# Kernel tuning notes

Measured on AMD Instinct MI355X. Metric: run time of the kernel, lower is better.

The kernel has to match this reference:

```python
import jax, jax.numpy as jnp
import numpy as np

N_NODES = 50000
N_EDGES = 800000
NUM_FEATURES = 128
HIDDEN = 128
NUM_CLASSES = 10
NUM_GRAPHS = 512
PROCESSING_STEPS = 4


def setup_inputs() -> dict:
    key = jax.random.key(0)
    ks = jax.random.split(key, 20)
    s = 0.05
    inp = {
        'x': jax.random.normal(ks[0], (N_NODES, NUM_FEATURES), jnp.float32),
        'edge_index': jax.random.randint(ks[1], (2, N_EDGES), 0, N_NODES),
        'batch': jnp.sort(jax.random.randint(ks[2], (N_NODES,), 0, NUM_GRAPHS)),
        # GCN layers (weights stored [in, out])
        'W1': jax.random.normal(ks[3], (NUM_FEATURES, HIDDEN), jnp.float32) * s,
        'b1': jnp.zeros((HIDDEN,), jnp.float32),
        'W2': jax.random.normal(ks[4], (HIDDEN, HIDDEN), jnp.float32) * s,
        'b2': jnp.zeros((HIDDEN,), jnp.float32),
        'W3': jax.random.normal(ks[5], (HIDDEN, HIDDEN), jnp.float32) * s,
        'b3': jnp.zeros((HIDDEN,), jnp.float32),
        # Set2Set LSTM cell: input 2*HIDDEN -> hidden HIDDEN, torch gate order i,f,g,o
        'Wih': jax.random.normal(ks[6], (4 * HIDDEN, 2 * HIDDEN), jnp.float32) * s,
        'Whh': jax.random.normal(ks[7], (4 * HIDDEN, HIDDEN), jnp.float32) * s,
        'bih': jnp.zeros((4 * HIDDEN,), jnp.float32),
        'bhh': jnp.zeros((4 * HIDDEN,), jnp.float32),
        # MLP head
        'L1w': jax.random.normal(ks[8], (2 * HIDDEN, HIDDEN), jnp.float32) * s,
        'L1b': jnp.zeros((HIDDEN,), jnp.float32),
        'L2w': jax.random.normal(ks[9], (HIDDEN, HIDDEN // 2), jnp.float32) * s,
        'L2b': jnp.zeros((HIDDEN // 2,), jnp.float32),
        'L3w': jax.random.normal(ks[10], (HIDDEN // 2, NUM_CLASSES), jnp.float32) * s,
        'L3b': jnp.zeros((NUM_CLASSES,), jnp.float32),
    }
    return inp


def _gcn_conv(x, row, col, W, b, n):
    # PyG GCNConv: x @ W, symmetric normalization with self-loops, scatter-add to targets.
    xw = x @ W  # [N, out]
    deg = jax.ops.segment_sum(jnp.ones_like(col, dtype=xw.dtype), col, num_segments=n)
    dis = jnp.where(deg > 0, jax.lax.rsqrt(jnp.maximum(deg, 1.0)), 0.0)
    norm = dis[row] * dis[col]  # [E+N]
    out = jax.ops.segment_sum(norm[:, None] * xw[row], col, num_segments=n)
    return out + b


def _segment_softmax(e, batch, n_seg):
    emax = jax.lax.stop_gradient(jax.ops.segment_max(e, batch, num_segments=n_seg))
    emax = jnp.where(jnp.isfinite(emax), emax, 0.0)
    a = jnp.exp(e - emax[batch])
    asum = jax.ops.segment_sum(a, batch, num_segments=n_seg)
    return a / jnp.where(asum > 0, asum, 1.0)[batch]


def reference(x, edge_index, batch, W1, b1, W2, b2, W3, b3,
              Wih, Whh, bih, bhh, L1w, L1b, L2w, L2b, L3w, L3b):
    n = x.shape[0]
    # add self loops once
    loops = jnp.arange(n, dtype=edge_index.dtype)
    row = jnp.concatenate([edge_index[0], loops])  # sources
    col = jnp.concatenate([edge_index[1], loops])  # targets

    h = jax.nn.relu(_gcn_conv(x, row, col, W1, b1, n))
    h = jax.nn.relu(_gcn_conv(h, row, col, W2, b2, n))
    h = jax.nn.relu(_gcn_conv(h, row, col, W3, b3, n))

    # Set2Set readout (processing_steps=4)
    d = h.shape[1]
    hs = jnp.zeros((NUM_GRAPHS, d), h.dtype)
    cs = jnp.zeros((NUM_GRAPHS, d), h.dtype)
    q_star = jnp.zeros((NUM_GRAPHS, 2 * d), h.dtype)
    for _ in range(PROCESSING_STEPS):
        gates = q_star @ Wih.T + hs @ Whh.T + bih + bhh  # [B, 4d]
        ig, fg, gg, og = jnp.split(gates, 4, axis=-1)
        cs = jax.nn.sigmoid(fg) * cs + jax.nn.sigmoid(ig) * jnp.tanh(gg)
        q = jax.nn.sigmoid(og) * jnp.tanh(cs)
        hs = q
        e = jnp.sum(h * q[batch], axis=-1)  # [N]
        a = _segment_softmax(e, batch, NUM_GRAPHS)
        r = jax.ops.segment_sum(a[:, None] * h, batch, num_segments=NUM_GRAPHS)
        q_star = jnp.concatenate([q, r], axis=-1)

    # MLP head (dropout inactive in eval)
    y = jax.nn.relu(q_star @ L1w + L1b)
    y = jax.nn.relu(y @ L2w + L2b)
    y = y @ L3w + L3b
    return jax.nn.log_softmax(y, axis=-1)
```

## Files before the change

kernel.cpp:

```cpp
#include <hip/hip_runtime.h>

constexpr int NN  = 50000;
constexpr int NE  = 800000;
constexpr int FD  = 128;
constexpr int NG  = 512;
constexpr int NB  = 4;
constexpr int BCAP = 24;
constexpr int CAP = NB * BCAP;
constexpr int SLICE = 12500;
constexpr int NBKT   = 196;
constexpr int BNODES = 256;
constexpr int CAPB   = 6144;

typedef __attribute__((ext_vector_type(8))) short bf16x8;
typedef __attribute__((ext_vector_type(4))) float f32x4;

__device__ __forceinline__ float bf2f(unsigned short u) {
    unsigned int v = ((unsigned int)u) << 16;
    float f; __builtin_memcpy(&f, &v, 4); return f;
}
__device__ __forceinline__ unsigned short f2bf(float f) {
    unsigned int u; __builtin_memcpy(&u, &f, 4);
    u += 0x7FFFu + ((u >> 16) & 1u);
    return (unsigned short)(u >> 16);
}
__device__ __forceinline__ float2 bfp(unsigned int u) {
    unsigned int lo = u << 16, hi = u & 0xFFFF0000u;
    float2 r; __builtin_memcpy(&r.x, &lo, 4); __builtin_memcpy(&r.y, &hi, 4);
    return r;
}
__device__ __forceinline__ unsigned int packbf(float a, float b) {
    return (unsigned int)f2bf(a) | ((unsigned int)f2bf(b) << 16);
}
__device__ __forceinline__ float sigmoidf(float x) { return 1.0f / (1.0f + __expf(-x)); }
__device__ __forceinline__ float ldw(const void* p, int idx, int flag) {
    return flag ? ((const float*)p)[idx] : bf2f(((const unsigned short*)p)[idx]);
}

__global__ void k_detect(const unsigned int* __restrict__ xw, int* __restrict__ flag,
                         int* __restrict__ gcnt) {
    if (threadIdx.x < NBKT) gcnt[threadIdx.x] = 0;
    __shared__ int cnt;
    if (threadIdx.x == 0) cnt = 0;
    __syncthreads();
    int local = 0;
    for (int i = threadIdx.x; i < 2048; i += 256) {
        unsigned int w = xw[i];
        unsigned int h0 = w & 0xFFFFu, h1 = w >> 16;
        if (((h0 >> 7) & 0xFF) >= 0x90) local++;
        if (((h1 >> 7) & 0xFF) >= 0x90) local++;
    }
    atomicAdd(&cnt, local);
    __syncthreads();
    if (threadIdx.x == 0) *flag = (cnt > 256) ? 1 : 0;
}

__global__ void k_cvt_x(const void* __restrict__ src, unsigned short* __restrict__ dst,
                        const int* __restrict__ batch, int* __restrict__ goff,
                        const int* __restrict__ flagp) {
    int i = blockIdx.x * 256 + threadIdx.x;
    if (i < NN * FD / 8) {
        if (*flagp) {
            const float4* s = (const float4*)src;
            float4 a = s[2 * i], b = s[2 * i + 1];
            uint4 o;
            o.x = packbf(a.x, a.y); o.y = packbf(a.z, a.w);
            o.z = packbf(b.x, b.y); o.w = packbf(b.z, b.w);
            ((uint4*)dst)[i] = o;
        } else {
            ((uint4*)dst)[i] = ((const uint4*)src)[i];
        }
    }
    if (i < NN) {
        int b = batch[i];
        if (b < 0) b = 0;
        if (b >= NG) b = NG - 1;
        int prev;
        if (i == 0) prev = -1;
        else {
            prev = batch[i - 1];
            if (prev < 0) prev = 0;
            if (prev >= NG) prev = NG - 1;
        }
        for (int g = prev + 1; g <= b; g++) goff[g] = i;
        if (i == NN - 1)
            for (int g = b + 1; g <= NG; g++) goff[g] = NN;
    }
}

struct WDesc {
    const void* src[12];
    void* dst[12];
    int kind[12];
    int off[13];
};
__global__ void k_cvt_w(WDesc d, const int* __restrict__ flagp) {
    int gid = blockIdx.x * 256 + threadIdx.x;
    if (gid >= d.off[12]) return;
    int flag = *flagp;
    int t = 0;
    while (gid >= d.off[t + 1]) t++;
    int i = gid - d.off[t];
    if (d.kind[t] == 0) {
        if (flag) ((unsigned short*)d.dst[t])[i] = f2bf(((const float*)d.src[t])[i]);
        else      ((unsigned short*)d.dst[t])[i] = ((const unsigned short*)d.src[t])[i];
    } else {
        int n = i >> 6, k2 = i & 63;
        ((unsigned int*)d.dst[t])[i] = packbf(ldw(d.src[t], (2 * k2) * 128 + n, flag),
                                              ldw(d.src[t], (2 * k2 + 1) * 128 + n, flag));
    }
}

__global__ void k_wt(const void* __restrict__ Wih, const void* __restrict__ Whh,
                     const void* __restrict__ bih, const void* __restrict__ bhh,
                     unsigned int* __restrict__ WcombT,
                     unsigned int* __restrict__ WrT,
                     float* __restrict__ bsum, const int* __restrict__ flagp) {
    int gid = blockIdx.x * 256 + threadIdx.x;
    int flag = *flagp;
    if (gid < 64 * 512) {
        int k2 = gid >> 9, row = gid & 511;
        float a0 = ldw(Wih, row * 256 + 2 * k2, flag)     + ldw(Whh, row * 128 + 2 * k2, flag);
        float a1 = ldw(Wih, row * 256 + 2 * k2 + 1, flag) + ldw(Whh, row * 128 + 2 * k2 + 1, flag);
        WcombT[(k2 >> 1) * 1024 + 2 * row + (k2 & 1)] = packbf(a0, a1);
    } else if (gid < 2 * 64 * 512) {
        int g2 = gid - 64 * 512;
        int k2 = g2 >> 9, row = g2 & 511;
        WrT[(k2 >> 1) * 1024 + 2 * row + (k2 & 1)] =
            packbf(ldw(Wih, row * 256 + 128 + 2 * k2, flag),
                   ldw(Wih, row * 256 + 128 + 2 * k2 + 1, flag));
    } else if (gid < 2 * 64 * 512 + 512) {
        int row = gid - 2 * 64 * 512;
        bsum[row] = ldw(bih, row, flag) + ldw(bhh, row, flag);
    }
}

__global__ __launch_bounds__(256) void k_fill1(const int* __restrict__ ei,
                                               int* __restrict__ gcnt,
                                               unsigned int* __restrict__ bktbuf) {
    __shared__ int hist[NBKT];
    __shared__ int wbase[NBKT];
    int t = threadIdx.x;
    for (int i = t; i < NBKT; i += 256) hist[i] = 0;
    __syncthreads();
    int base_e = blockIdx.x * 2048;
    int bb[8], rk[8];
    unsigned int pk[8];
#pragma unroll
    for (int k = 0; k < 8; k++) {
        int e = base_e + k * 256 + t;
        if (e < NE) {
            int r = ei[e], c = ei[NE + e];
            if ((unsigned)r >= (unsigned)NN) r = 0;
            if ((unsigned)c >= (unsigned)NN) c = 0;
            bb[k] = c >> 8;
            rk[k] = atomicAdd(&hist[bb[k]], 1);
            pk[k] = ((unsigned)c << 16) | (unsigned)r;
        } else bb[k] = -1;
    }
    __syncthreads();
    for (int i = t; i < NBKT; i += 256)
        wbase[i] = hist[i] ? atomicAdd(&gcnt[i], hist[i]) : 0;
    __syncthreads();
#pragma unroll
    for (int k = 0; k < 8; k++) {
        if (bb[k] >= 0) {
            int pos = wbase[bb[k]] + rk[k];
            if (pos < CAPB) bktbuf[bb[k] * CAPB + pos] = pk[k];
        }
    }
}

__global__ __launch_bounds__(512) void k_fill2(const unsigned int* __restrict__ bktbuf,
                                               const int* __restrict__ gcnt,
                                               int* __restrict__ bcnt,
                                               unsigned short* __restrict__ csr_row) {
    int b = blockIdx.x, t = threadIdx.x;
    __shared__ int lcnt[BNODES * NB];
    for (int i = t; i < BNODES * NB; i += 512) lcnt[i] = 0;
    uint4* creg = (uint4*)(csr_row + (size_t)b * BNODES * CAP);
    for (int i = t; i < BNODES * CAP / 8; i += 512)
        creg[i] = (uint4){0, 0, 0, 0};
    __syncthreads();
    int n = gcnt[b]; if (n > CAPB) n = CAPB;
    const unsigned int* bp = bktbuf + (size_t)b * CAPB;
    for (int i = t; i < n; i += 512) {
        unsigned int v = bp[i];
        int r = v & 0xFFFFu;
        int c = v >> 16;
        int cl = c & (BNODES - 1);
        int nb = r / SLICE;
        int pos = atomicAdd(&lcnt[cl * NB + nb], 1);
        if (pos < BCAP)
            csr_row[(size_t)c * CAP + nb * BCAP + pos] = (unsigned short)r;
    }
    __syncthreads();
    for (int i = t; i < BNODES * NB; i += 512) {
        int node = b * BNODES + (i >> 2);
        if (node < NN) bcnt[(size_t)node * NB + (i & 3)] = lcnt[i];
    }
}

__global__ __launch_bounds__(256) void k_gemm(const unsigned short* __restrict__ H,
                                              const unsigned int* __restrict__ WT,
                                              const int4* __restrict__ bcnt4,
                                              unsigned short* __restrict__ XW, int M) {
    __shared__ alignas(16) unsigned short WB[128 * 136];
    int t = threadIdx.x;
    unsigned int* WBu = (unsigned int*)WB;
    for (int c = t; c < 2048; c += 256) {
        uint4 v = ((const uint4*)WT)[c];
        int n = c >> 4, k2q = c & 15;
        *(uint4*)(WBu + n * 68 + k2q * 4) = v;
    }
    __syncthreads();
    int wave = t >> 6, lane = t & 63;
    int lm = lane & 15;
    int lq = lane >> 4;
    int row = blockIdx.x * 64 + wave * 16 + lm;
    int rowc = (row < M) ? row : (M - 1);
    const unsigned short* Arow = H + (size_t)rowc * 128;
    f32x4 acc[8];
#pragma unroll
    for (int n = 0; n < 8; n++) acc[n] = (f32x4){0.f, 0.f, 0.f, 0.f};
#pragma unroll
    for (int kk = 0; kk < 4; kk++) {
        bf16x8 afrag = *(const bf16x8*)(Arow + kk * 32 + lq * 8);
        const unsigned short* wbase = WB + kk * 32 + lq * 8;
#pragma unroll
        for (int n = 0; n < 8; n++) {
            bf16x8 bfrag = *(const bf16x8*)(wbase + (n * 16 + lm) * 136);
            acc[n] = __builtin_amdgcn_mfma_f32_16x16x32_bf16(afrag, bfrag, acc[n], 0, 0, 0);
        }
    }
    __syncthreads();
#pragma unroll
    for (int r = 0; r < 4; r++) {
        int row_local = wave * 16 + lq * 4 + r;
        int orow = blockIdx.x * 64 + row_local;
        int oc = (orow < M) ? orow : (M - 1);
        int4 bc = bcnt4[oc];
        float dn = rsqrtf((float)(bc.x + bc.y + bc.z + bc.w + 1));
#pragma unroll
        for (int n = 0; n < 8; n++)
            WB[row_local * 136 + n * 16 + lm] = f2bf(acc[n][r] * dn);
    }
#pragma unroll
    for (int it = 0; it < 4; it++) {
        int row_local = wave * 16 + it * 4 + (lane >> 4);
        int row_global = blockIdx.x * 64 + row_local;
        uint4 v = *(const uint4*)(WB + row_local * 136 + (lane & 15) * 8);
        if (row_global < M)
            *((uint4*)(XW + (size_t)row_global * 128) + (lane & 15)) = v;
    }
}

__global__ __launch_bounds__(256) void k_aggr(const unsigned short* __restrict__ XW,
                                              const int4* __restrict__ bcnt4,
                                              const unsigned short* __restrict__ csr_row,
                                              const unsigned short* __restrict__ bias,
                                              unsigned short* __restrict__ Hout) {
    int wave = threadIdx.x >> 6;
    int lane = threadIdx.x & 63;
    int nsel = lane >> 4;
    int sub  = lane & 15;
    int node = blockIdx.x * 16 + wave * 4 + nsel;
    if (node >= NN) return;
    const uint4* XW4 = (const uint4*)XW;
    int4 bc = bcnt4[node];
    int deg = bc.x + bc.y + bc.z + bc.w;
    float dn = rsqrtf((float)(deg + 1));
    uint4 sv = XW4[(size_t)node * 16 + sub];
    float2 s0 = bfp(sv.x), s1 = bfp(sv.y), s2 = bfp(sv.z), s3 = bfp(sv.w);
    float a0 = s0.x, a1 = s0.y, a2 = s1.x, a3 = s1.y;
    float a4 = s2.x, a5 = s2.y, a6 = s3.x, a7 = s3.y;
    int cnts[NB] = {bc.x, bc.y, bc.z, bc.w};
    const unsigned short* lst = csr_row + (size_t)node * CAP;
#pragma unroll
    for (int b = 0; b < NB; b++) {
        int n = cnts[b]; if (n > BCAP) n = BCAP;
        const unsigned short* lb = lst + b * BCAP;
        int j = 0;
        for (; j + 4 <= n; j += 4) {
            int r0 = lb[j], r1 = lb[j + 1], r2 = lb[j + 2], r3 = lb[j + 3];
            uint4 v0 = XW4[(size_t)r0 * 16 + sub];
            uint4 v1 = XW4[(size_t)r1 * 16 + sub];
            uint4 v2 = XW4[(size_t)r2 * 16 + sub];
            uint4 v3 = XW4[(size_t)r3 * 16 + sub];
            float2 f;
            f = bfp(v0.x); a0 += f.x; a1 += f.y;
            f = bfp(v0.y); a2 += f.x; a3 += f.y;
            f = bfp(v0.z); a4 += f.x; a5 += f.y;
            f = bfp(v0.w); a6 += f.x; a7 += f.y;
            f = bfp(v1.x); a0 += f.x; a1 += f.y;
            f = bfp(v1.y); a2 += f.x; a3 += f.y;
            f = bfp(v1.z); a4 += f.x; a5 += f.y;
            f = bfp(v1.w); a6 += f.x; a7 += f.y;
            f = bfp(v2.x); a0 += f.x; a1 += f.y;
            f = bfp(v2.y); a2 += f.x; a3 += f.y;
            f = bfp(v2.z); a4 += f.x; a5 += f.y;
            f = bfp(v2.w); a6 += f.x; a7 += f.y;
            f = bfp(v3.x); a0 += f.x; a1 += f.y;
            f = bfp(v3.y); a2 += f.x; a3 += f.y;
            f = bfp(v3.z); a4 += f.x; a5 += f.y;
            f = bfp(v3.w); a6 += f.x; a7 += f.y;
        }
        for (; j < n; j++) {
            int r = lb[j];
            uint4 v = XW4[(size_t)r * 16 + sub];
            float2 f;
            f = bfp(v.x); a0 += f.x; a1 += f.y;
            f = bfp(v.y); a2 += f.x; a3 += f.y;
            f = bfp(v.z); a4 += f.x; a5 += f.y;
            f = bfp(v.w); a6 += f.x; a7 += f.y;
        }
    }
    uint4 bv = ((const uint4*)bias)[sub];
    float2 b0 = bfp(bv.x), b1 = bfp(bv.y), b2 = bfp(bv.z), b3 = bfp(bv.w);
    uint4 o;
    o.x = packbf(fmaxf(dn * a0 + b0.x, 0.0f), fmaxf(dn * a1 + b0.y, 0.0f));
    o.y = packbf(fmaxf(dn * a2 + b1.x, 0.0f), fmaxf(dn * a3 + b1.y, 0.0f));
    o.z = packbf(fmaxf(dn * a4 + b2.x, 0.0f), fmaxf(dn * a5 + b2.y, 0.0f));
    o.w = packbf(fmaxf(dn * a6 + b3.x, 0.0f), fmaxf(dn * a7 + b3.y, 0.0f));
    ((uint4*)Hout)[(size_t)node * 16 + sub] = o;
}

__global__ __launch_bounds__(512) void k_s2s(const unsigned short* __restrict__ H,
                                             const int* __restrict__ goff,
                                             const unsigned int* __restrict__ WcombT,
                                             const unsigned int* __restrict__ WrT,
                                             const float* __restrict__ bsum,
                                             const unsigned short* __restrict__ L1w,
                                             const unsigned short* __restrict__ L1b,
                                             const unsigned short* __restrict__ L2w,
                                             const unsigned short* __restrict__ L2b,
                                             const unsigned short* __restrict__ L3w,
                                             const unsigned short* __restrict__ L3b,
                                             void* __restrict__ out,
                                             const int* __restrict__ flagp) {
    int g = blockIdx.x, t = threadIdx.x;
    __shared__ float qsr[256];
    __shared__ float hsv[128], csv[128];
    __shared__ float gates[512];
    __shared__ float wred[8];
    __shared__ float wrr[8][128];
    __shared__ float ps[128];
    __shared__ float qrep[4 * 132];
    __shared__ float y1[128], y2[64], y3[10], lseS[1];

    if (t < 256) qsr[t] = 0.0f;
    if (t < 128) { hsv[t] = 0.0f; csv[t] = 0.0f; }
    __syncthreads();

    int s = goff[g], e = goff[g + 1];
    if (s < 0) s = 0;
    if (e > NN) e = NN;
    if (e < s) e = s;
    int w = t >> 6, lane = t & 63;
    const unsigned int* Hu = (const unsigned int*)H;

    int nq = t >> 2;
    int fq = (t & 3) * 16;
    const float* qc = qrep + (t & 3) * 132 + 2 * fq;
    const uint2* WC2 = (const uint2*)WcombT;
    const uint2* WR2 = (const uint2*)WrT;

    for (int step = 0; step < 4; step++) {
        {
            float accA = bsum[t], accB = 0.0f, accC = 0.0f, accD = 0.0f;
#pragma unroll 8
            for (int p = 0; p < 32; p++) {
                uint2 u = WC2[p * 512 + t];
                float2 w0 = bfp(u.x), w1 = bfp(u.y);
                accA += w0.x * hsv[4 * p];     accB += w0.y * hsv[4 * p + 1];
                accC += w1.x * hsv[4 * p + 2]; accD += w1.y * hsv[4 * p + 3];
            }
#pragma unroll 8
            for (int p = 0; p < 32; p++) {
                uint2 u = WR2[p * 512 + t];
                float2 w0 = bfp(u.x), w1 = bfp(u.y);
                accA += w0.x * qsr[128 + 4 * p];     accB += w0.y * qsr[128 + 4 * p + 1];
                accC += w1.x * qsr[128 + 4 * p + 2]; accD += w1.y * qsr[128 + 4 * p + 3];
            }
            gates[t] = (accA + accB) + (accC + accD);
        }
        __syncthreads();
        if (t < 128) {
            float ig = sigmoidf(gates[t]),       fg = sigmoidf(gates[128 + t]);
            float gg = tanhf(gates[256 + t]),    og = sigmoidf(gates[384 + t]);
            float c = fg * csv[t] + ig * gg;
            float q = og * tanhf(c);
            csv[t] = c;
            hsv[t] = q;
            qsr[t] = q;
            qrep[t] = q; qrep[132 + t] = q; qrep[264 + t] = q; qrep[396 + t] = q;
        }
        __syncthreads();

        float m = -1e30f, l = 0.0f, r0 = 0.0f, r1 = 0.0f;
        for (int cs = s; cs < e; cs += 128) {
            int ce = cs + 128; if (ce > e) ce = e;
            int nid = cs + nq;
            float eacc = 0.0f;
            if (nid < ce) {
                const unsigned int* hrow = Hu + (size_t)nid * 64 + fq;
#pragma unroll
                for (int u = 0; u < 16; u += 4) {
                    uint4 hv = *(const uint4*)(hrow + u);
                    float2 f0 = bfp(hv.x), f1 = bfp(hv.y);
                    float2 f2 = bfp(hv.z), f3 = bfp(hv.w);
                    const float* qp = qc + 2 * u;
                    eacc += f0.x * qp[0] + f0.y * qp[1] + f1.x * qp[2] + f1.y * qp[3]
                          + f2.x * qp[4] + f2.y * qp[5] + f3.x * qp[6] + f3.y * qp[7];
                }
            }
            eacc += __shfl_xor(eacc, 1);
            eacc += __shfl_xor(eacc, 2);
            float esc = (nid < ce) ? eacc : -1e30f;
            float vmax = esc;
            for (int d = 4; d < 64; d <<= 1) vmax = fmaxf(vmax, __shfl_xor(vmax, d));
            if (lane == 0) wred[w] = vmax;
            __syncthreads();
            float M = m;
#pragma unroll
            for (int k = 0; k < 8; k++) M = fmaxf(M, wred[k]);
            float p = __expf(esc - M);
            bool lead = ((t & 3) == 0) && (nid < ce);
            if (lead) ps[nq] = p;
            float psum = lead ? p : 0.0f;
            for (int d = 1; d < 64; d <<= 1) psum += __shfl_xor(psum, d);
            __syncthreads();
            if (lane == 0) wred[w] = psum;
            __syncthreads();
            float Lc = 0.0f;
#pragma unroll
            for (int k = 0; k < 8; k++) Lc += wred[k];
            float scale = __expf(m - M);
            l = l * scale + Lc;
            r0 *= scale; r1 *= scale;
            m = M;
            int i = cs + w;
            for (; i + 24 < ce; i += 32) {
                float p0 = ps[i - cs],      p1 = ps[i + 8 - cs];
                float p2 = ps[i + 16 - cs], p3 = ps[i + 24 - cs];
                unsigned int v0 = Hu[(size_t)i * 64 + lane];
                unsigned int v1 = Hu[(size_t)(i + 8) * 64 + lane];
                unsigned int v2 = Hu[(size_t)(i + 16) * 64 + lane];
                unsigned int v3 = Hu[(size_t)(i + 24) * 64 + lane];
                float2 f0 = bfp(v0), f1 = bfp(v1), f2 = bfp(v2), f3 = bfp(v3);
                r0 += p0 * f0.x + p1 * f1.x + p2 * f2.x + p3 * f3.x;
                r1 += p0 * f0.y + p1 * f1.y + p2 * f2.y + p3 * f3.y;
            }
            for (; i < ce; i += 8) {
                float p0 = ps[i - cs];
                float2 f = bfp(Hu[(size_t)i * 64 + lane]);
                r0 += p0 * f.x; r1 += p0 * f.y;
            }
            __syncthreads();
        }
        wrr[w][2 * lane]     = r0;
        wrr[w][2 * lane + 1] = r1;
        __syncthreads();
        if (t < 128) {
            float R = 0.0f;
#pragma unroll
            for (int k = 0; k < 8; k++) R += wrr[k][t];
            float L = l;
            if (!(L > 0.0f)) L = 1.0f;
            qsr[128 + t] = R / L;
        }
        __syncthreads();
    }

    if (t < 128) {
        float acc = bf2f(L1b[t]);
        for (int i = 0; i < 256; i++) acc += bf2f(L1w[i * 128 + t]) * qsr[i];
        y1[t] = fmaxf(acc, 0.0f);
    }
    __syncthreads();
    if (t < 64) {
        float a2 = bf2f(L2b[t]);
        for (int i = 0; i < 128; i++) a2 += bf2f(L2w[i * 64 + t]) * y1[i];
        y2[t] = fmaxf(a2, 0.0f);
    }
    __syncthreads();
    if (t < 10) {
        float a3 = bf2f(L3b[t]);
        for (int i = 0; i < 64; i++) a3 += bf2f(L3w[i * 10 + t]) * y2[i];
        y3[t] = a3;
    }
    __syncthreads();
    if (t == 0) {
        float m = y3[0];
        for (int i = 1; i < 10; i++) m = fmaxf(m, y3[i]);
        float s2 = 0.0f;
        for (int i = 0; i < 10; i++) s2 += __expf(y3[i] - m);
        lseS[0] = m + __logf(s2);
    }
    __syncthreads();
    if (t < 10) {
        float v = y3[t] - lseS[0];
        if (!(v == v)) v = -9.0f;
        if (*flagp) ((float*)out)[g * 10 + t] = v;
        else        ((unsigned short*)out)[g * 10 + t] = f2bf(v);
    }
}

extern "C" void kernel_launch(void* const* d_in, const int* in_sizes, int n_in,
                              void* d_out, int out_size, void* d_ws, size_t ws_size,
                              hipStream_t stream) {
    const int* ei  = (const int*)d_in[1];
    const int* bat = (const int*)d_in[2];

    char* base = (char*)d_ws;
    size_t woff = 0;
    auto alloc = [&](size_t bytes) -> void* {
        void* r = base + woff;
        woff = (woff + bytes + 255) & ~(size_t)255;
        return r;
    };
    unsigned short* A = (unsigned short*)alloc((size_t)NN * FD * 2);
    unsigned short* B = (unsigned short*)alloc((size_t)NN * FD * 2);
    unsigned short* csr_row = (unsigned short*)alloc((size_t)NBKT * BNODES * CAP * 2);
    int*   bcnt     = (int*)alloc((size_t)NN * NB * 4);
    int*   goff     = (int*)alloc((NG + 1) * 4);
    int*   flag     = (int*)alloc(256);
    int*   gcnt     = (int*)alloc(NBKT * 4);
    unsigned int* WcombT = (unsigned int*)alloc(64 * 512 * 4);
    unsigned int* WrT    = (unsigned int*)alloc(64 * 512 * 4);
    float* bsum          = (float*)alloc(512 * 4);
    unsigned int* cWT1 = (unsigned int*)alloc(8192 * 4);
    unsigned int* cWT2 = (unsigned int*)alloc(8192 * 4);
    unsigned int* cWT3 = (unsigned int*)alloc(8192 * 4);
    auto walloc = [&](int n) { return (unsigned short*)alloc((size_t)n * 2); };
    unsigned short* cb1  = walloc(128);
    unsigned short* cb2  = walloc(128);
    unsigned short* cb3  = walloc(128);
    unsigned short* cL1w = walloc(256 * 128);
    unsigned short* cL1b = walloc(128);
    unsigned short* cL2w = walloc(128 * 64);
    unsigned short* cL2b = walloc(64);
    unsigned short* cL3w = walloc(64 * 10);
    unsigned short* cL3b = walloc(10);
    unsigned int* bktbuf = (unsigned int*)A;
    (void)ws_size; (void)in_sizes; (void)n_in; (void)out_size;

    k_detect<<<1, 256, 0, stream>>>((const unsigned int*)d_in[0], flag, gcnt);
    k_cvt_x<<<(NN * FD / 8 + 255) / 256, 256, 0, stream>>>(d_in[0], B, bat, goff, flag);
    {
        WDesc d;
        const int idxs[12]  = {3,    4,  5,    6,  7,    8,  13, 14, 15, 16, 17, 18};
        void* dsts[12]      = {cWT1, cb1, cWT2, cb2, cWT3, cb3,
                               cL1w, cL1b, cL2w, cL2b, cL3w, cL3b};
        const int kinds[12] = {1, 0, 1, 0, 1, 0, 0, 0, 0, 0, 0, 0};
        const int ns[12]    = {8192, 128, 8192, 128, 8192, 128,
                               256 * 128, 128, 128 * 64, 64, 64 * 10, 10};
        int acc = 0;
        for (int i = 0; i < 12; i++) {
            d.src[i] = d_in[idxs[i]];
            d.dst[i] = dsts[i];
            d.kind[i] = kinds[i];
            d.off[i] = acc;
            acc += ns[i];
        }
        d.off[12] = acc;
        k_cvt_w<<<(acc + 255) / 256, 256, 0, stream>>>(d, flag);
    }
    k_wt<<<(2 * 64 * 512 + 512 + 255) / 256, 256, 0, stream>>>(
        d_in[9], d_in[10], d_in[11], d_in[12], WcombT, WrT, bsum, flag);

    k_fill1<<<(NE + 2047) / 2048, 256, 0, stream>>>(ei, gcnt, bktbuf);
    k_fill2<<<NBKT, 512, 0, stream>>>(bktbuf, gcnt, bcnt, csr_row);

    const int gemmBlk = (NN + 63) / 64;
    const int aggrBlk = (NN + 15) / 16;

    k_gemm<<<gemmBlk, 256, 0, stream>>>(B, cWT1, (const int4*)bcnt, A, NN);
    k_aggr<<<aggrBlk, 256, 0, stream>>>(A, (const int4*)bcnt, csr_row, cb1, B);
    k_gemm<<<gemmBlk, 256, 0, stream>>>(B, cWT2, (const int4*)bcnt, A, NN);
    k_aggr<<<aggrBlk, 256, 0, stream>>>(A, (const int4*)bcnt, csr_row, cb2, B);
    k_gemm<<<gemmBlk, 256, 0, stream>>>(B, cWT3, (const int4*)bcnt, A, NN);
    k_aggr<<<aggrBlk, 256, 0, stream>>>(A, (const int4*)bcnt, csr_row, cb3, B);

    k_s2s<<<NG, 512, 0, stream>>>(B, goff, WcombT, WrT, bsum,
                                  cL1w, cL1b, cL2w, cL2b, cL3w, cL3b,
                                  d_out, flag);
}
```

Baseline: 319.9 us.

## Merge weight-conversion kernels, cache LSTM weights in registers, trim s2s barriers

Folds the k_cvt_w weight conversion into k_wt so one launch does both, saving a kernel launch. In the Set2Set kernel, 24 of the 32 combined-gate weight vectors are held in registers across the four processing steps instead of being reloaded from global memory each step. The softmax max and sum reductions now use separate shared slots, which removes one barrier, and the trailing barrier in the chunk loop runs only when another chunk follows. The register caching raises register pressure at 512 threads per block, which may cost occupancy.

Result: slower. 336.9 us (+5.3%).

```diff
diff --git a/kernel.cpp b/kernel.cpp
--- a/kernel.cpp
+++ b/kernel.cpp
@@ -94,28 +94,12 @@
     int kind[12];
     int off[13];
 };
-__global__ void k_cvt_w(WDesc d, const int* __restrict__ flagp) {
-    int gid = blockIdx.x * 256 + threadIdx.x;
-    if (gid >= d.off[12]) return;
-    int flag = *flagp;
-    int t = 0;
-    while (gid >= d.off[t + 1]) t++;
-    int i = gid - d.off[t];
-    if (d.kind[t] == 0) {
-        if (flag) ((unsigned short*)d.dst[t])[i] = f2bf(((const float*)d.src[t])[i]);
-        else      ((unsigned short*)d.dst[t])[i] = ((const unsigned short*)d.src[t])[i];
-    } else {
-        int n = i >> 6, k2 = i & 63;
-        ((unsigned int*)d.dst[t])[i] = packbf(ldw(d.src[t], (2 * k2) * 128 + n, flag),
-                                              ldw(d.src[t], (2 * k2 + 1) * 128 + n, flag));
-    }
-}
-
 __global__ void k_wt(const void* __restrict__ Wih, const void* __restrict__ Whh,
                      const void* __restrict__ bih, const void* __restrict__ bhh,
                      unsigned int* __restrict__ WcombT,
                      unsigned int* __restrict__ WrT,
-                     float* __restrict__ bsum, const int* __restrict__ flagp) {
+                     float* __restrict__ bsum, WDesc d,
+                     const int* __restrict__ flagp) {
     int gid = blockIdx.x * 256 + threadIdx.x;
     int flag = *flagp;
     if (gid < 64 * 512) {
@@ -132,6 +116,19 @@
     } else if (gid < 2 * 64 * 512 + 512) {
         int row = gid - 2 * 64 * 512;
         bsum[row] = ldw(bih, row, flag) + ldw(bhh, row, flag);
+    }
+    if (gid < d.off[12]) {
+        int t = 0;
+        while (gid >= d.off[t + 1]) t++;
+        int i = gid - d.off[t];
+        if (d.kind[t] == 0) {
+            if (flag) ((unsigned short*)d.dst[t])[i] = f2bf(((const float*)d.src[t])[i]);
+            else      ((unsigned short*)d.dst[t])[i] = ((const unsigned short*)d.src[t])[i];
+        } else {
+            int n = i >> 6, k2 = i & 63;
+            ((unsigned int*)d.dst[t])[i] = packbf(ldw(d.src[t], (2 * k2) * 128 + n, flag),
+                                                  ldw(d.src[t], (2 * k2 + 1) * 128 + n, flag));
+        }
     }
 }
 
@@ -342,7 +339,7 @@
     __shared__ float qsr[256];
     __shared__ float hsv[128], csv[128];
     __shared__ float gates[512];
-    __shared__ float wred[8];
+    __shared__ float wredM[8], wredS[8];
     __shared__ float wrr[8][128];
     __shared__ float ps[128];
     __shared__ float qrep[4 * 132];
@@ -365,11 +362,21 @@
     const uint2* WC2 = (const uint2*)WcombT;
     const uint2* WR2 = (const uint2*)WrT;
 
+    uint2 wc[24];
+#pragma unroll
+    for (int p = 0; p < 24; p++) wc[p] = WC2[p * 512 + t];
+
     for (int step = 0; step < 4; step++) {
         {
             float accA = bsum[t], accB = 0.0f, accC = 0.0f, accD = 0.0f;
-#pragma unroll 8
-            for (int p = 0; p < 32; p++) {
+#pragma unroll
+            for (int p = 0; p < 24; p++) {
+                float2 w0 = bfp(wc[p].x), w1 = bfp(wc[p].y);
+                accA += w0.x * hsv[4 * p];     accB += w0.y * hsv[4 * p + 1];
+                accC += w1.x * hsv[4 * p + 2]; accD += w1.y * hsv[4 * p + 3];
+            }
+#pragma unroll
+            for (int p = 24; p < 32; p++) {
                 uint2 u = WC2[p * 512 + t];
                 float2 w0 = bfp(u.x), w1 = bfp(u.y);
                 accA += w0.x * hsv[4 * p];     accB += w0.y * hsv[4 * p + 1];
@@ -419,22 +426,21 @@
             float esc = (nid < ce) ? eacc : -1e30f;
             float vmax = esc;
             for (int d = 4; d < 64; d <<= 1) vmax = fmaxf(vmax, __shfl_xor(vmax, d));
-            if (lane == 0) wred[w] = vmax;
+            if (lane == 0) wredM[w] = vmax;
             __syncthreads();
             float M = m;
 #pragma unroll
-            for (int k = 0; k < 8; k++) M = fmaxf(M, wred[k]);
+            for (int k = 0; k < 8; k++) M = fmaxf(M, wredM[k]);
             float p = __expf(esc - M);
             bool lead = ((t & 3) == 0) && (nid < ce);
             if (lead) ps[nq] = p;
             float psum = lead ? p : 0.0f;
             for (int d = 1; d < 64; d <<= 1) psum += __shfl_xor(psum, d);
-            __syncthreads();
-            if (lane == 0) wred[w] = psum;
+            if (lane == 0) wredS[w] = psum;
             __syncthreads();
             float Lc = 0.0f;
 #pragma unroll
-            for (int k = 0; k < 8; k++) Lc += wred[k];
+            for (int k = 0; k < 8; k++) Lc += wredS[k];
             float scale = __expf(m - M);
             l = l * scale + Lc;
             r0 *= scale; r1 *= scale;
@@ -456,7 +462,7 @@
                 float2 f = bfp(Hu[(size_t)i * 64 + lane]);
                 r0 += p0 * f.x; r1 += p0 * f.y;
             }
-            __syncthreads();
+            if (ce < e) __syncthreads();
         }
         wrr[w][2 * lane]     = r0;
         wrr[w][2 * lane + 1] = r1;
@@ -564,10 +570,10 @@
             acc += ns[i];
         }
         d.off[12] = acc;
-        k_cvt_w<<<(acc + 255) / 256, 256, 0, stream>>>(d, flag);
-    }
-    k_wt<<<(2 * 64 * 512 + 512 + 255) / 256, 256, 0, stream>>>(
-        d_in[9], d_in[10], d_in[11], d_in[12], WcombT, WrT, bsum, flag);
+        int work = (2 * 64 * 512 + 512 > acc) ? (2 * 64 * 512 + 512) : acc;
+        k_wt<<<(work + 255) / 256, 256, 0, stream>>>(
+            d_in[9], d_in[10], d_in[11], d_in[12], WcombT, WrT, bsum, d, flag);
+    }
 
     k_fill1<<<(NE + 2047) / 2048, 256, 0, stream>>>(ei, gcnt, bktbuf);
     k_fill2<<<NBKT, 512, 0, stream>>>(bktbuf, gcnt, bcnt, csr_row);
```
